# Performance work log

Measured on AMD Instinct MI355X. Metric: run time of the kernel, lower is better.

## Reference

```python
import jax, jax.numpy as jnp
import numpy as np

B, E, D, O, K = 16384, 8, 1024, 1024, 2  # tokens, experts, d_model, output_size, top_k


def setup_inputs() -> dict:
    key = jax.random.key(0)
    kx, kl, kw = jax.random.split(key, 3)
    x = jax.random.normal(kx, (B, D), jnp.float32)
    # Sparse top-k gates: softmax over top-k logits, zeros elsewhere (the
    # structure SparseDispatcher assumes: (gates > 0) marks routed tokens).
    logits = jax.random.normal(kl, (B, E), jnp.float32)
    vals, idx = jax.lax.top_k(logits, K)              # [B,K]
    w = jax.nn.softmax(vals, axis=-1)
    gates = jnp.zeros((B, E), jnp.float32).at[jnp.arange(B)[:, None], idx].set(w)
    # Per-expert Linear weights/biases (nn.Linear(expert_sizes[i], output_size)).
    W = jax.random.normal(kw, (E, D, O), jnp.float32) / np.sqrt(D)
    b = jnp.zeros((E, O), jnp.float32)
    return {"x": x, "gates": gates, "W": W, "b": b}


def reference(x, gates, W, b):
    """MoE dispatch -> per-expert Linear -> gated combine.

    Mathematically identical to: for each expert e, gather tokens with
    gates[:, e] > 0, apply Linear_e, multiply by the gate value, and
    scatter-sum back to [B, O]. Expressed densely per expert (gate values
    are exactly zero for non-routed tokens), which keeps it jit-friendly.
    """
    out = jnp.zeros((x.shape[0], W.shape[-1]), x.dtype)
    for e in range(W.shape[0]):  # small fixed expert count
        out = out + (x @ W[e] + b[e]) * gates[:, e, None]
    return out
```

## Files before the change

### kernel.cpp

```cpp
#include <hip/hip_runtime.h>
#include <hip/hip_bf16.h>


#define TOK 16384
#define DD  1024
#define OO  1024
#define NE  8
#define NBIN 64
#define MAXT 168
#define BM  160
#define BN  128
#define BK  64

typedef __bf16 bf16x8 __attribute__((ext_vector_type(8)));
typedef float  f32x4  __attribute__((ext_vector_type(4)));

__device__ __forceinline__ unsigned short f2bf(float f) {
  unsigned u = __float_as_uint(f);
  u += 0x7fffu + ((u >> 16) & 1u);
  return (unsigned short)(u >> 16);
}

__device__ __forceinline__ void gload_lds16(const void* g, void* l) {
  __builtin_amdgcn_global_load_lds(
      (const __attribute__((address_space(1))) void*)g,
      (__attribute__((address_space(3))) void*)l, 16, 0, 0);
}

#define PREP_ROUTE_B 64
#define PREP_CVTX_B  4096
#define PREP_CVTW_B  2048

__global__ __launch_bounds__(256) void prep(
    const float* __restrict__ x, const float* __restrict__ gates,
    const float* __restrict__ W,
    unsigned short* __restrict__ xs, unsigned short* __restrict__ wtb,
    int* __restrict__ cnt, int* __restrict__ idx, float2* __restrict__ gp) {
  __shared__ float tile[64][65];
  int bid = blockIdx.x;

  if (bid < PREP_ROUTE_B) {
    __shared__ int h[NBIN];
    __shared__ int gbase[NBIN];
    if (threadIdx.x < NBIN) h[threadIdx.x] = 0;
    __syncthreads();
    int i = bid * 256 + threadIdx.x;
    int e1 = -1, e2 = -1; float g1 = 0.f, g2 = 0.f;
#pragma unroll
    for (int e = 0; e < NE; ++e) {
      float g = gates[i * NE + e];
      if (g > 0.f) { if (e1 < 0) { e1 = e; g1 = g; } else if (e2 < 0) { e2 = e; g2 = g; } }
    }
    float r, s; int pid = 0, rank = 0, valid = (e1 >= 0);
    if (valid) {
      if (e2 < 0) { e2 = e1; r = 1.f; s = 0.5f * g1; }
      else        { r = g1 / g2; s = g2; }
      pid = e1 * NE + e2;
      rank = atomicAdd(&h[pid], 1);
    } else { r = 0.f; s = 0.f; }
    __syncthreads();
    if (threadIdx.x < NBIN && h[threadIdx.x] > 0)
      gbase[threadIdx.x] = atomicAdd(cnt + threadIdx.x, h[threadIdx.x]);
    __syncthreads();
    if (valid) {
      int pos = gbase[pid] + rank;
      idx[pid * TOK + pos] = i;
      gp[(size_t)pid * TOK + pos] = make_float2(r, s);
    }

  } else if (bid < PREP_ROUTE_B + PREP_CVTX_B) {
    size_t base = (size_t)(bid - PREP_ROUTE_B) * 1024 + threadIdx.x;
    const float4* xp = (const float4*)x;
#pragma unroll
    for (int q = 0; q < 4; ++q) {
      float4 v = xp[base + q * 256];
      alignas(8) unsigned short o4[4] = {f2bf(v.x), f2bf(v.y), f2bf(v.z), f2bf(v.w)};
      *(uint2*)(xs + (base + q * 256) * 4) = *(const uint2*)o4;
    }

  } else {
    int wb = bid - (PREP_ROUTE_B + PREP_CVTX_B);
    int e = wb >> 8, tt = wb & 255;
    int d0 = (tt >> 4) * 64, o0 = (tt & 15) * 64;
    const float* src = W + ((size_t)e << 20) + (size_t)d0 * OO + o0;
    for (int i = threadIdx.x; i < 1024; i += 256) {
      int r = i >> 4, c4 = (i & 15) * 4;
      float4 v = *(const float4*)(src + (size_t)r * OO + c4);
      tile[r][c4 + 0] = v.x; tile[r][c4 + 1] = v.y;
      tile[r][c4 + 2] = v.z; tile[r][c4 + 3] = v.w;
    }
    __syncthreads();
    unsigned short* dst = wtb + ((size_t)e << 20) + (size_t)o0 * DD + d0;
    for (int i = threadIdx.x; i < 512; i += 256) {
      int o = i >> 3, d8 = (i & 7) * 8;
      alignas(16) unsigned short w8[8];
#pragma unroll
      for (int j = 0; j < 8; ++j) w8[j] = f2bf(tile[d8 + j][o]);
      *(uint4*)(dst + (size_t)o * DD + d8) = *(const uint4*)w8;
    }
  }
}

__global__ __launch_bounds__(256) void moe_gemm(
    const unsigned short* __restrict__ xs,
    const unsigned short* __restrict__ wtb, const int* __restrict__ idx,
    const float2* __restrict__ gp, const int* __restrict__ cnt,
    const float* __restrict__ bias, float* __restrict__ out) {
  __shared__ unsigned short As[2 * BM * BK];
  __shared__ unsigned short Bs[2 * BN * BK];
  __shared__ int    rowsS[BM];
  __shared__ float2 gS[BM];
  __shared__ int    sPid, sLt, sCnt;

  if (threadIdx.x < 64) {
    int lane = threadIdx.x;
    if (lane == 0) sPid = -1;
    int c = cnt[lane];
    int n = (c + BM - 1) / BM;
    int pre = n;
#pragma unroll
    for (int o = 1; o < 64; o <<= 1) {
      int v = __shfl_up(pre, o);
      if (lane >= o) pre += v;
    }
    int lo = pre - n;
    int tb = blockIdx.x;
    if (tb >= lo && tb < pre) { sPid = lane; sLt = tb - lo; sCnt = c; }
  }
  __syncthreads();
  int pid = sPid;
  if (pid < 0) return;
  int lt = sLt, cntv = sCnt;
  int e1 = pid >> 3, e2 = pid & 7;
  int n0 = blockIdx.y * BN;

  int t = threadIdx.x, lane = t & 63, w = t >> 6;
  if (t < BM) {
    int slot = lt * BM + t;
    int tok = 0; float2 g = make_float2(0.f, 0.f);
    if (slot < cntv) { tok = idx[pid * TOK + slot]; g = gp[(size_t)pid * TOK + slot]; }
    rowsS[t] = tok; gS[t] = g;
  }
  __syncthreads();

  const unsigned short* aP[5];
  const unsigned short* bP[4];
  int csrc = (((lane & 7) ^ (lane >> 3)) << 3);
#pragma unroll
  for (int it = 0; it < 5; ++it) {
    int r = (w * 5 + it) * 8 + (lane >> 3);
    aP[it] = xs + (size_t)rowsS[r] * DD + csrc;
  }
#pragma unroll
  for (int it = 0; it < 4; ++it) {
    int r = (w * 4 + it) * 8 + (lane >> 3);
    bP[it] = wtb + ((size_t)e1 * OO + n0 + r) * DD + csrc;
  }
  const ptrdiff_t bAdv = (ptrdiff_t)(e2 - e1) * OO * DD;

  int wm = w >> 1, wn = w & 1;
  int hi = lane >> 4, lo = lane & 15;
  int aOff[5][2], bOff[4][2];
#pragma unroll
  for (int m = 0; m < 5; ++m) {
    int arow = wm * 80 + m * 16 + lo;
#pragma unroll
    for (int ks = 0; ks < 2; ++ks)
      aOff[m][ks] = arow * BK + ((((ks << 2) + hi) ^ (arow & 7)) << 3);
  }
#pragma unroll
  for (int n = 0; n < 4; ++n) {
    int brow = wn * 64 + n * 16 + lo;
#pragma unroll
    for (int ks = 0; ks < 2; ++ks)
      bOff[n][ks] = brow * BK + ((((ks << 2) + hi) ^ (brow & 7)) << 3);
  }

  auto STAGE = [&](int g, int buf) {
    int k0 = (g & 15) << 6;
    int aB = buf * (BM * BK), bB = buf * (BN * BK);
    const ptrdiff_t badd = (g & 16) ? bAdv : 0;
#pragma unroll
    for (int it = 0; it < 5; ++it)
      gload_lds16(aP[it] + k0, As + aB + (((w * 5) + it) << 9));
#pragma unroll
    for (int it = 0; it < 4; ++it)
      gload_lds16(bP[it] + badd + k0, Bs + bB + (((w << 2) + it) << 9));
  };

  f32x4 acc[5][4] = {};

  STAGE(0, 0);
#pragma unroll 1
  for (int g = 0; g < 32; ++g) {
    int cur = g & 1;
    __syncthreads();
    if (g < 31) STAGE(g + 1, cur ^ 1);
    int aB = cur * (BM * BK), bB = cur * (BN * BK);
#pragma unroll
    for (int ks = 0; ks < 2; ++ks) {
      bf16x8 af[5], bfr[4];
#pragma unroll
      for (int m = 0; m < 5; ++m) af[m] = *(const bf16x8*)(As + aB + aOff[m][ks]);
#pragma unroll
      for (int n = 0; n < 4; ++n) bfr[n] = *(const bf16x8*)(Bs + bB + bOff[n][ks]);
#pragma unroll
      for (int m = 0; m < 5; ++m)
#pragma unroll
        for (int n = 0; n < 4; ++n)
          acc[m][n] = __builtin_amdgcn_mfma_f32_16x16x32_bf16(af[m], bfr[n], acc[m][n], 0, 0, 0);
    }
    if (g == 15) {
#pragma unroll
      for (int m = 0; m < 5; ++m) {
        float rr[4];
#pragma unroll
        for (int j = 0; j < 4; ++j) rr[j] = gS[wm * 80 + m * 16 + hi * 4 + j].x;
#pragma unroll
        for (int n = 0; n < 4; ++n)
#pragma unroll
          for (int j = 0; j < 4; ++j) acc[m][n][j] *= rr[j];
      }
    }
  }

  const float* b1 = bias + e1 * OO;
  const float* b2 = bias + e2 * OO;
  float b1v[4], b2v[4];
#pragma unroll
  for (int n = 0; n < 4; ++n) {
    int col = n0 + wn * 64 + n * 16 + lo;
    b1v[n] = b1[col]; b2v[n] = b2[col];
  }
#pragma unroll
  for (int m = 0; m < 5; ++m) {
#pragma unroll
    for (int j = 0; j < 4; ++j) {
      int rl = wm * 80 + m * 16 + hi * 4 + j;
      int slot = lt * BM + rl;
      if (slot < cntv) {
        float2 g = gS[rl];
        float* orow = out + (size_t)rowsS[rl] * OO + n0 + wn * 64 + lo;
#pragma unroll
        for (int n = 0; n < 4; ++n)
          orow[n * 16] = g.y * (acc[m][n][j] + g.x * b1v[n] + b2v[n]);
      }
    }
  }
}

extern "C" void kernel_launch(void* const* d_in, const int* in_sizes, int n_in,
                              void* d_out, int out_size, void* d_ws, size_t ws_size,
                              hipStream_t stream) {
  const float* x     = (const float*)d_in[0];
  const float* gates = (const float*)d_in[1];
  const float* W     = (const float*)d_in[2];
  const float* bias  = (const float*)d_in[3];
  float* out = (float*)d_out;

  char* ws = (char*)d_ws;
  size_t off = 0;
  unsigned short* xs  = (unsigned short*)(ws + off); off += (size_t)TOK * DD * 2;
  unsigned short* wtb = (unsigned short*)(ws + off); off += (size_t)NE * DD * OO * 2;
  int*    idx  = (int*)(ws + off);    off += (size_t)NBIN * TOK * 4;
  float2* gp   = (float2*)(ws + off); off += (size_t)NBIN * TOK * 8;
  int*    cnt  = (int*)(ws + off);    off += NBIN * 4;
  if (ws_size < off) return;

  hipMemsetAsync(cnt, 0, NBIN * 4, stream);
  prep<<<PREP_ROUTE_B + PREP_CVTX_B + PREP_CVTW_B, 256, 0, stream>>>(
      x, gates, W, xs, wtb, cnt, idx, gp);
  dim3 gg(MAXT, OO / BN, 1);
  moe_gemm<<<gg, 256, 0, stream>>>(xs, wtb, idx, gp, cnt, bias, out);
}
```

Before: 127.9 us.

## Retile MoE GEMM to 128x256 with 512 threads and 4-deep LDS pipeline

Reworks the expert GEMM kernel to use 128x256 output tiles with 8 waves and a K step of 32 split across four LDS buffers, keeping three stages of loads in flight. Synchronisation is now explicit, using vmcnt waits, raw barriers and sched_barrier, and MFMA sections run at raised priority. The aim is better overlap of global-to-LDS loads with matrix math and more reuse of each loaded tile. The cost is a larger LDS footprint (96 KB per block) and more tiles per expert pair because BM drops to 128. The barrier and waitcnt choreography is also fragile.

```diff
diff --git a/kernel.cpp b/kernel.cpp
--- a/kernel.cpp
+++ b/kernel.cpp
@@ -7,10 +7,12 @@
 #define OO  1024
 #define NE  8
 #define NBIN 64
-#define MAXT 168
-#define BM  160
-#define BN  128
-#define BK  64
+#define MAXT 192
+#define BM  128
+#define BN  256
+#define BKH 32
+#define A_HALF (BM * BKH)
+#define B_HALF (BN * BKH)
 
 typedef __bf16 bf16x8 __attribute__((ext_vector_type(8)));
 typedef float  f32x4  __attribute__((ext_vector_type(4)));
@@ -26,6 +28,12 @@
       (const __attribute__((address_space(1))) void*)g,
       (__attribute__((address_space(3))) void*)l, 16, 0, 0);
 }
+
+#define ENDP(N) do { \
+    asm volatile("s_waitcnt vmcnt(" #N ")" ::: "memory"); \
+    __builtin_amdgcn_s_barrier(); \
+    __builtin_amdgcn_sched_barrier(0); \
+  } while (0)
 
 #define PREP_ROUTE_B 64
 #define PREP_CVTX_B  4096
@@ -101,13 +109,13 @@
   }
 }
 
-__global__ __launch_bounds__(256) void moe_gemm(
+__global__ __launch_bounds__(512, 2) void moe_gemm(
     const unsigned short* __restrict__ xs,
     const unsigned short* __restrict__ wtb, const int* __restrict__ idx,
     const float2* __restrict__ gp, const int* __restrict__ cnt,
     const float* __restrict__ bias, float* __restrict__ out) {
-  __shared__ unsigned short As[2 * BM * BK];
-  __shared__ unsigned short Bs[2 * BN * BK];
+  __shared__ unsigned short As[4 * A_HALF];
+  __shared__ unsigned short Bs[4 * B_HALF];
   __shared__ int    rowsS[BM];
   __shared__ float2 gS[BM];
   __shared__ int    sPid, sLt, sCnt;
@@ -116,7 +124,7 @@
     int lane = threadIdx.x;
     if (lane == 0) sPid = -1;
     int c = cnt[lane];
-    int n = (c + BM - 1) / BM;
+    int n = (c + BM - 1) >> 7;
     int pre = n;
 #pragma unroll
     for (int o = 1; o < 64; o <<= 1) {
@@ -143,86 +151,78 @@
   }
   __syncthreads();
 
-  const unsigned short* aP[5];
-  const unsigned short* bP[4];
-  int csrc = (((lane & 7) ^ (lane >> 3)) << 3);
-#pragma unroll
-  for (int it = 0; it < 5; ++it) {
-    int r = (w * 5 + it) * 8 + (lane >> 3);
-    aP[it] = xs + (size_t)rowsS[r] * DD + csrc;
-  }
-#pragma unroll
-  for (int it = 0; it < 4; ++it) {
-    int r = (w * 4 + it) * 8 + (lane >> 3);
-    bP[it] = wtb + ((size_t)e1 * OO + n0 + r) * DD + csrc;
-  }
-  const ptrdiff_t bAdv = (ptrdiff_t)(e2 - e1) * OO * DD;
-
-  int wm = w >> 1, wn = w & 1;
+  int srcChunk = (((lane & 3) ^ ((lane >> 3) & 3)) << 3);
+  int rA = w * 16 + (lane >> 2);
+  const unsigned short* aSrc = xs + (size_t)rowsS[rA] * DD + srcChunk;
+  int rB = w * 32 + (lane >> 2);
+  const unsigned short* bSrc = wtb + ((size_t)e1 * OO + n0 + rB) * DD + srcChunk;
+  const ptrdiff_t bAdvE = (ptrdiff_t)(e2 - e1) * OO * DD;
+
+  int wm = w >> 2, wn = w & 3;
   int hi = lane >> 4, lo = lane & 15;
-  int aOff[5][2], bOff[4][2];
-#pragma unroll
-  for (int m = 0; m < 5; ++m) {
-    int arow = wm * 80 + m * 16 + lo;
-#pragma unroll
-    for (int ks = 0; ks < 2; ++ks)
-      aOff[m][ks] = arow * BK + ((((ks << 2) + hi) ^ (arow & 7)) << 3);
-  }
-#pragma unroll
-  for (int n = 0; n < 4; ++n) {
-    int brow = wn * 64 + n * 16 + lo;
-#pragma unroll
-    for (int ks = 0; ks < 2; ++ks)
-      bOff[n][ks] = brow * BK + ((((ks << 2) + hi) ^ (brow & 7)) << 3);
-  }
-
-  auto STAGE = [&](int g, int buf) {
-    int k0 = (g & 15) << 6;
-    int aB = buf * (BM * BK), bB = buf * (BN * BK);
-    const ptrdiff_t badd = (g & 16) ? bAdv : 0;
-#pragma unroll
-    for (int it = 0; it < 5; ++it)
-      gload_lds16(aP[it] + k0, As + aB + (((w * 5) + it) << 9));
-#pragma unroll
-    for (int it = 0; it < 4; ++it)
-      gload_lds16(bP[it] + badd + k0, Bs + bB + (((w << 2) + it) << 9));
+  int swz = ((hi ^ ((lo >> 1) & 3)) << 3);
+  int aOff[4], bOff[4];
+#pragma unroll
+  for (int m = 0; m < 4; ++m) aOff[m] = (wm * 64 + m * 16 + lo) * BKH + swz;
+#pragma unroll
+  for (int n = 0; n < 4; ++n) bOff[n] = (wn * 64 + n * 16 + lo) * BKH + swz;
+
+  f32x4 acc[4][4] = {};
+
+  auto STAGE = [&](int h) {
+    int hb = h & 3;
+    size_t ko = (size_t)(h & 31) * BKH;
+    const unsigned short* a = aSrc + ko;
+    const unsigned short* b = bSrc + ko + ((h >= 32) ? bAdvE : (ptrdiff_t)0);
+    gload_lds16(a, (unsigned short*)As + hb * A_HALF + w * 512);
+    gload_lds16(b, (unsigned short*)Bs + hb * B_HALF + w * 1024);
+    gload_lds16(b + (size_t)16 * DD, (unsigned short*)Bs + hb * B_HALF + w * 1024 + 512);
   };
 
-  f32x4 acc[5][4] = {};
-
-  STAGE(0, 0);
+  auto PHASE = [&](int h, bool stg) {
+    if (stg) STAGE(h + 3);
+    int hb = h & 3;
+    const unsigned short* Ab = As + hb * A_HALF;
+    const unsigned short* Bb = Bs + hb * B_HALF;
+    bf16x8 af[4], bv[4];
+#pragma unroll
+    for (int m = 0; m < 4; ++m) af[m] = *(const bf16x8*)(Ab + aOff[m]);
+#pragma unroll
+    for (int n = 0; n < 4; ++n) bv[n] = *(const bf16x8*)(Bb + bOff[n]);
+    __builtin_amdgcn_s_barrier();
+    asm volatile("s_waitcnt lgkmcnt(0)" ::: "memory");
+    __builtin_amdgcn_sched_barrier(0);
+    __builtin_amdgcn_s_setprio(1);
+#pragma unroll
+    for (int m = 0; m < 4; ++m)
+#pragma unroll
+      for (int n = 0; n < 4; ++n)
+        acc[m][n] = __builtin_amdgcn_mfma_f32_16x16x32_bf16(af[m], bv[n], acc[m][n], 0, 0, 0);
+    __builtin_amdgcn_s_setprio(0);
+    __builtin_amdgcn_sched_barrier(0);
+  };
+
+  STAGE(0); STAGE(1); STAGE(2);
+  ENDP(6);
+
 #pragma unroll 1
-  for (int g = 0; g < 32; ++g) {
-    int cur = g & 1;
-    __syncthreads();
-    if (g < 31) STAGE(g + 1, cur ^ 1);
-    int aB = cur * (BM * BK), bB = cur * (BN * BK);
-#pragma unroll
-    for (int ks = 0; ks < 2; ++ks) {
-      bf16x8 af[5], bfr[4];
-#pragma unroll
-      for (int m = 0; m < 5; ++m) af[m] = *(const bf16x8*)(As + aB + aOff[m][ks]);
-#pragma unroll
-      for (int n = 0; n < 4; ++n) bfr[n] = *(const bf16x8*)(Bs + bB + bOff[n][ks]);
-#pragma unroll
-      for (int m = 0; m < 5; ++m)
-#pragma unroll
-        for (int n = 0; n < 4; ++n)
-          acc[m][n] = __builtin_amdgcn_mfma_f32_16x16x32_bf16(af[m], bfr[n], acc[m][n], 0, 0, 0);
-    }
-    if (g == 15) {
-#pragma unroll
-      for (int m = 0; m < 5; ++m) {
-        float rr[4];
-#pragma unroll
-        for (int j = 0; j < 4; ++j) rr[j] = gS[wm * 80 + m * 16 + hi * 4 + j].x;
-#pragma unroll
-        for (int n = 0; n < 4; ++n)
-#pragma unroll
-          for (int j = 0; j < 4; ++j) acc[m][n][j] *= rr[j];
-      }
-    }
-  }
+  for (int h = 0; h < 31; ++h) { PHASE(h, true); ENDP(6); }
+  PHASE(31, true); ENDP(6);
+#pragma unroll
+  for (int m = 0; m < 4; ++m) {
+    float rr[4];
+#pragma unroll
+    for (int j = 0; j < 4; ++j) rr[j] = gS[wm * 64 + m * 16 + hi * 4 + j].x;
+#pragma unroll
+    for (int n = 0; n < 4; ++n)
+#pragma unroll
+      for (int j = 0; j < 4; ++j) acc[m][n][j] *= rr[j];
+  }
+#pragma unroll 1
+  for (int h = 32; h <= 60; ++h) { PHASE(h, true); ENDP(6); }
+  PHASE(61, false); ENDP(3);
+  PHASE(62, false); ENDP(0);
+  PHASE(63, false);
 
   const float* b1 = bias + e1 * OO;
   const float* b2 = bias + e2 * OO;
@@ -233,10 +233,10 @@
     b1v[n] = b1[col]; b2v[n] = b2[col];
   }
 #pragma unroll
-  for (int m = 0; m < 5; ++m) {
+  for (int m = 0; m < 4; ++m) {
 #pragma unroll
     for (int j = 0; j < 4; ++j) {
-      int rl = wm * 80 + m * 16 + hi * 4 + j;
+      int rl = wm * 64 + m * 16 + hi * 4 + j;
       int slot = lt * BM + rl;
       if (slot < cntv) {
         float2 g = gS[rl];
@@ -271,5 +271,5 @@
   prep<<<PREP_ROUTE_B + PREP_CVTX_B + PREP_CVTW_B, 256, 0, stream>>>(
       x, gates, W, xs, wtb, cnt, idx, gp);
   dim3 gg(MAXT, OO / BN, 1);
-  moe_gemm<<<gg, 256, 0, stream>>>(xs, wtb, idx, gp, cnt, bias, out);
-}
+  moe_gemm<<<gg, 512, 0, stream>>>(xs, wtb, idx, gp, cnt, bias, out);
+}
```

New measurement: 200.5 us. +56.8%, slower.

## Switch MoE GEMM to 128x256 tile with single-buffered LDS

Applied to the files above, without the earlier changes.

Changes the grouped GEMM tile from 160x128 to 128x256, with each of the four waves covering all 128 rows and a 64-column slice, which raises per-wave accumulator work to 8x4 MFMA tiles. It also drops LDS double buffering: each k-step now loads, syncs, computes and syncs again, with no overlap between global-to-LDS loads and MFMA work. The larger N tile halves the number of column blocks and cuts redundant A-gather traffic, but it raises register pressure and exposes load latency. Padding waste per expert-pair bin also changes.

```diff
diff --git a/kernel.cpp b/kernel.cpp
--- a/kernel.cpp
+++ b/kernel.cpp
@@ -7,9 +7,9 @@
 #define OO  1024
 #define NE  8
 #define NBIN 64
-#define MAXT 168
-#define BM  160
-#define BN  128
+#define MAXT 192
+#define BM  128
+#define BN  256
 #define BK  64
 
 typedef __bf16 bf16x8 __attribute__((ext_vector_type(8)));
@@ -106,8 +106,8 @@
     const unsigned short* __restrict__ wtb, const int* __restrict__ idx,
     const float2* __restrict__ gp, const int* __restrict__ cnt,
     const float* __restrict__ bias, float* __restrict__ out) {
-  __shared__ unsigned short As[2 * BM * BK];
-  __shared__ unsigned short Bs[2 * BN * BK];
+  __shared__ unsigned short As[BM * BK];
+  __shared__ unsigned short Bs[BN * BK];
   __shared__ int    rowsS[BM];
   __shared__ float2 gS[BM];
   __shared__ int    sPid, sLt, sCnt;
@@ -116,7 +116,7 @@
     int lane = threadIdx.x;
     if (lane == 0) sPid = -1;
     int c = cnt[lane];
-    int n = (c + BM - 1) / BM;
+    int n = (c + BM - 1) >> 7;
     int pre = n;
 #pragma unroll
     for (int o = 1; o < 64; o <<= 1) {
@@ -143,85 +143,77 @@
   }
   __syncthreads();
 
-  const unsigned short* aP[5];
-  const unsigned short* bP[4];
+  const unsigned short* aP[4];
+  const unsigned short* bP[8];
   int csrc = (((lane & 7) ^ (lane >> 3)) << 3);
-#pragma unroll
-  for (int it = 0; it < 5; ++it) {
-    int r = (w * 5 + it) * 8 + (lane >> 3);
-    aP[it] = xs + (size_t)rowsS[r] * DD + csrc;
-  }
 #pragma unroll
   for (int it = 0; it < 4; ++it) {
     int r = (w * 4 + it) * 8 + (lane >> 3);
+    aP[it] = xs + (size_t)rowsS[r] * DD + csrc;
+  }
+#pragma unroll
+  for (int it = 0; it < 8; ++it) {
+    int r = (w * 8 + it) * 8 + (lane >> 3);
     bP[it] = wtb + ((size_t)e1 * OO + n0 + r) * DD + csrc;
   }
   const ptrdiff_t bAdv = (ptrdiff_t)(e2 - e1) * OO * DD;
 
-  int wm = w >> 1, wn = w & 1;
   int hi = lane >> 4, lo = lane & 15;
-  int aOff[5][2], bOff[4][2];
-#pragma unroll
-  for (int m = 0; m < 5; ++m) {
-    int arow = wm * 80 + m * 16 + lo;
+  int aOff[8][2], bOff[4][2];
+#pragma unroll
+  for (int m = 0; m < 8; ++m) {
+    int arow = m * 16 + lo;
 #pragma unroll
     for (int ks = 0; ks < 2; ++ks)
       aOff[m][ks] = arow * BK + ((((ks << 2) + hi) ^ (arow & 7)) << 3);
   }
 #pragma unroll
   for (int n = 0; n < 4; ++n) {
-    int brow = wn * 64 + n * 16 + lo;
+    int brow = w * 64 + n * 16 + lo;
 #pragma unroll
     for (int ks = 0; ks < 2; ++ks)
       bOff[n][ks] = brow * BK + ((((ks << 2) + hi) ^ (brow & 7)) << 3);
   }
 
-  auto STAGE = [&](int g, int buf) {
-    int k0 = (g & 15) << 6;
-    int aB = buf * (BM * BK), bB = buf * (BN * BK);
-    const ptrdiff_t badd = (g & 16) ? bAdv : 0;
-#pragma unroll
-    for (int it = 0; it < 5; ++it)
-      gload_lds16(aP[it] + k0, As + aB + (((w * 5) + it) << 9));
-#pragma unroll
-    for (int it = 0; it < 4; ++it)
-      gload_lds16(bP[it] + badd + k0, Bs + bB + (((w << 2) + it) << 9));
-  };
-
-  f32x4 acc[5][4] = {};
-
-  STAGE(0, 0);
+  f32x4 acc[8][4] = {};
+
 #pragma unroll 1
   for (int g = 0; g < 32; ++g) {
-    int cur = g & 1;
-    __syncthreads();
-    if (g < 31) STAGE(g + 1, cur ^ 1);
-    int aB = cur * (BM * BK), bB = cur * (BN * BK);
+    int k0 = (g & 15) << 6;
+    const ptrdiff_t badd = (g & 16) ? bAdv : 0;
+#pragma unroll
+    for (int it = 0; it < 4; ++it)
+      gload_lds16(aP[it] + k0, As + (((w << 2) + it) << 9));
+#pragma unroll
+    for (int it = 0; it < 8; ++it)
+      gload_lds16(bP[it] + badd + k0, Bs + (((w << 3) + it) << 9));
+    __syncthreads();
 #pragma unroll
     for (int ks = 0; ks < 2; ++ks) {
-      bf16x8 af[5], bfr[4];
-#pragma unroll
-      for (int m = 0; m < 5; ++m) af[m] = *(const bf16x8*)(As + aB + aOff[m][ks]);
-#pragma unroll
-      for (int n = 0; n < 4; ++n) bfr[n] = *(const bf16x8*)(Bs + bB + bOff[n][ks]);
-#pragma unroll
-      for (int m = 0; m < 5; ++m)
+      bf16x8 af[8], bfr[4];
+#pragma unroll
+      for (int m = 0; m < 8; ++m) af[m] = *(const bf16x8*)(As + aOff[m][ks]);
+#pragma unroll
+      for (int n = 0; n < 4; ++n) bfr[n] = *(const bf16x8*)(Bs + bOff[n][ks]);
+#pragma unroll
+      for (int m = 0; m < 8; ++m)
 #pragma unroll
         for (int n = 0; n < 4; ++n)
           acc[m][n] = __builtin_amdgcn_mfma_f32_16x16x32_bf16(af[m], bfr[n], acc[m][n], 0, 0, 0);
     }
     if (g == 15) {
 #pragma unroll
-      for (int m = 0; m < 5; ++m) {
+      for (int m = 0; m < 8; ++m) {
         float rr[4];
 #pragma unroll
-        for (int j = 0; j < 4; ++j) rr[j] = gS[wm * 80 + m * 16 + hi * 4 + j].x;
+        for (int j = 0; j < 4; ++j) rr[j] = gS[m * 16 + hi * 4 + j].x;
 #pragma unroll
         for (int n = 0; n < 4; ++n)
 #pragma unroll
           for (int j = 0; j < 4; ++j) acc[m][n][j] *= rr[j];
       }
     }
+    __syncthreads();
   }
 
   const float* b1 = bias + e1 * OO;
@@ -229,18 +221,18 @@
   float b1v[4], b2v[4];
 #pragma unroll
   for (int n = 0; n < 4; ++n) {
-    int col = n0 + wn * 64 + n * 16 + lo;
+    int col = n0 + w * 64 + n * 16 + lo;
     b1v[n] = b1[col]; b2v[n] = b2[col];
   }
 #pragma unroll
-  for (int m = 0; m < 5; ++m) {
+  for (int m = 0; m < 8; ++m) {
 #pragma unroll
     for (int j = 0; j < 4; ++j) {
-      int rl = wm * 80 + m * 16 + hi * 4 + j;
+      int rl = m * 16 + hi * 4 + j;
       int slot = lt * BM + rl;
       if (slot < cntv) {
         float2 g = gS[rl];
-        float* orow = out + (size_t)rowsS[rl] * OO + n0 + wn * 64 + lo;
+        float* orow = out + (size_t)rowsS[rl] * OO + n0 + w * 64 + lo;
 #pragma unroll
         for (int n = 0; n < 4; ++n)
           orow[n * 16] = g.y * (acc[m][n][j] + g.x * b1v[n] + b2v[n]);
```

After: 188.3 us. 47.2% more time.
